# Optimization experiments

Measured on AMD Instinct MI355X. Metric: run time of the kernel, lower is better.

The kernel has to match this reference:

```python
import jax, jax.numpy as jnp
import numpy as np

B, N, G, H = 64, 1000, 500, 256
TANH_CLIP = 10.0


def setup_inputs() -> dict:
    key = jax.random.key(0)
    ks = jax.random.split(key, 8)
    embeddings = jax.random.normal(ks[0], (B, N, H), dtype=jnp.float32)
    dists = jax.random.uniform(ks[1], (B, N, N), dtype=jnp.float32)
    last_node = jax.random.randint(ks[2], (B, G), 0, N)
    visited = jax.random.uniform(ks[3], (B, G, N)) < 0.3
    group_ninf_mask = jnp.where(visited, -jnp.inf, 0.0).astype(jnp.float32)
    s = 1.0 / np.sqrt(H)
    Wq_graph = jax.random.normal(ks[4], (H, H), dtype=jnp.float32) * s
    Wq_first = jax.random.normal(ks[5], (H, H), dtype=jnp.float32) * s
    Wq_last = jax.random.normal(ks[6], (H, H), dtype=jnp.float32) * s
    W_visited = jax.random.normal(ks[7], (H, H), dtype=jnp.float32) * s
    return dict(embeddings=embeddings, dists=dists, last_node=last_node,
                group_ninf_mask=group_ninf_mask, Wq_graph=Wq_graph,
                Wq_first=Wq_first, Wq_last=Wq_last, W_visited=W_visited)


def reference(embeddings, dists, last_node, group_ninf_mask,
              Wq_graph, Wq_first, Wq_last, W_visited) -> jnp.ndarray:
    b, n, h = embeddings.shape
    g = last_node.shape[1]
    inv_sqrt_h = 1.0 / np.float32(np.sqrt(h))
    inv_sqrt_2 = np.float32(1.0 / np.sqrt(2.0))

    # reset(): graph query from mean-pooled embeddings  [B,1,H]
    q_graph = jnp.einsum('bih,oh->bio', embeddings.mean(axis=1, keepdims=True), Wq_graph)

    # gather last-node embeddings  [B,G,H]
    idx = jnp.broadcast_to(last_node[:, :, None], (b, g, h))
    last_emb = jnp.take_along_axis(embeddings, idx, axis=1)
    q_last = jnp.einsum('bgh,oh->bgo', last_emb, Wq_last)
    # first call: q_first built from the same last-node embedding
    q_first = jnp.einsum('bgh,oh->bgo', last_emb, Wq_first)

    # visited-set query: mask (-inf->1) @ embeddings / N, then linear
    mask_visited = jnp.where(jnp.isneginf(group_ninf_mask), 1.0, group_ninf_mask)
    pooled = jnp.einsum('bgn,bnh->bgh', mask_visited, embeddings) / np.float32(n)
    q_visited = jnp.einsum('bgh,oh->bgo', pooled, W_visited)

    # distances from last node to all nodes  [B,G,N]
    didx = jnp.broadcast_to(last_node[:, :, None], (b, g, n))
    distances = jnp.take_along_axis(dists, didx, axis=1)

    final_q = q_last + q_first + q_graph + q_visited  # [B,G,H]
    score = jnp.einsum('bgh,bnh->bgn', final_q, embeddings) * inv_sqrt_h - distances * inv_sqrt_2
    score_clipped = TANH_CLIP * jnp.tanh(score)
    mask_prob = jnp.where(jnp.isneginf(group_ninf_mask), -1e8, group_ninf_mask)
    return jax.nn.softmax(score_clipped + mask_prob, axis=-1)
```

## Files before the change

### kernel.cpp

```cpp
#include <hip/hip_runtime.h>
#include <hip/hip_fp16.h>
#include <math.h>

#define Bb 64
#define Nn 1000
#define Gg 500
#define Hh 256
#define GP 512
#define NP 1024

#define WS_QG   0u
#define WS_RS   16384u
#define WS_BM   49152u
#define WS_WC16 1097728u
#define WS_E16  1163264u
#define WS_T16  9355264u
#define WS_P16  17743872u
#define WS_F16  WS_T16
#define WS_PO   21938176u
#define WS_MP   38322176u

typedef __attribute__((ext_vector_type(8))) short short8;
typedef __attribute__((ext_vector_type(8))) _Float16 f16x8;
typedef __attribute__((ext_vector_type(4))) float f32x4;
typedef __attribute__((ext_vector_type(4))) unsigned short u16x4;

#define MFMAH(a,b,c) __builtin_amdgcn_mfma_f32_16x16x32_f16(a,b,c,0,0,0)
#define SW(row, chunk) (((row) << 6) + ((((chunk) ^ ((row) & 7))) << 3))

__device__ __forceinline__ unsigned short f16b(float v) {
  return __half_as_ushort(__float2half(v));
}

__global__ __launch_bounds__(256) void k_misc(const float* __restrict__ gm,
                                              const float* __restrict__ Wf,
                                              const float* __restrict__ Wl,
                                              const float* __restrict__ Wv,
                                              float* __restrict__ ws) {
  int bid = blockIdx.x, t = threadIdx.x;
  if (bid < 8192) {
    int w = t >> 6, l = t & 63;
    int row = bid * 4 + w;
    int b = row >> 9, g = row & 511;
    unsigned long long* dst = (unsigned long long*)((unsigned short*)(ws + WS_BM) + (size_t)row * 64);
    if (g < Gg) {
      const float* src = gm + ((size_t)b * Gg + g) * Nn;
#pragma unroll
      for (int i = 0; i < 16; ++i) {
        int n = i * 64 + l;
        bool bit = (n < Nn) ? (src[n] < -1e30f) : false;
        unsigned long long m = __ballot(bit);
        if (l == i) dst[i] = m;
      }
    } else {
      if (l < 16) dst[l] = 0ull;
    }
  } else if (bid < 8448) {
    int o = bid - 8192, k = t;
    unsigned short* wc = (unsigned short*)(ws + WS_WC16);
    wc[o*512 + k]       = f16b(Wv[o*Hh + k]);
    wc[o*512 + 256 + k] = f16b(Wl[o*Hh + k] + Wf[o*Hh + k]);
  } else {
    ws[WS_RS + (bid - 8448) * 256 + t] = 0.f;
  }
}

__global__ __launch_bounds__(256) void k_prep(const float* __restrict__ emb,
                                              float* __restrict__ ws) {
  __shared__ float tile[64][68];
  __shared__ float colsum[16][64];
  int nt = blockIdx.x, ht = blockIdx.y, b = blockIdx.z;
  int t = threadIdx.x;
  int c4 = (t & 15) * 4, r0 = t >> 4;
  int n0 = nt * 64, h0 = ht * 64;
  unsigned short* e16 = (unsigned short*)(ws + WS_E16);
  unsigned short* t16 = (unsigned short*)(ws + WS_T16);
  float cs0 = 0.f, cs1 = 0.f, cs2 = 0.f, cs3 = 0.f;
#pragma unroll
  for (int rr = 0; rr < 4; ++rr) {
    int r = r0 + rr * 16;
    int n = n0 + r;
    float4 v = {0.f, 0.f, 0.f, 0.f};
    if (n < Nn) {
      size_t idx = ((size_t)(b * Nn + n)) * Hh + h0 + c4;
      v = *(const float4*)(emb + idx);
      u16x4 e4 = { f16b(v.x), f16b(v.y), f16b(v.z), f16b(v.w) };
      *(u16x4*)(e16 + idx) = e4;
    }
    *(float4*)&tile[r][c4] = v;
    cs0 += v.x; cs1 += v.y; cs2 += v.z; cs3 += v.w;
  }
  colsum[r0][c4 + 0] = cs0; colsum[r0][c4 + 1] = cs1;
  colsum[r0][c4 + 2] = cs2; colsum[r0][c4 + 3] = cs3;
  __syncthreads();
  {
    int h_l = t >> 2, nseg = t & 3;
    short8 h8a, h8b;
#pragma unroll
    for (int i = 0; i < 16; ++i) {
      float v = tile[nseg * 16 + i][h_l];
      unsigned short hv = f16b(v);
      if (i < 8) h8a[i] = (short)hv;
      else       h8b[i-8] = (short)hv;
    }
    size_t base = ((size_t)(b * Hh + h0 + h_l)) * NP + n0 + nseg * 16;
    *(short8*)(t16 + base) = h8a; *(short8*)(t16 + base + 8) = h8b;
  }
  if (t < 64) {
    float s = 0.f;
#pragma unroll
    for (int i = 0; i < 16; ++i) s += colsum[i][t];
    ws[WS_MP + (((size_t)(b * Hh + h0 + t)) << 4) + nt] = s;
  }
}

__global__ __launch_bounds__(256) void k_qgraph(const float* __restrict__ Wg,
                                                float* __restrict__ ws) {
  __shared__ float mean[Hh];
  int b = blockIdx.x, t = threadIdx.x;
  {
    const float4* mp4 = (const float4*)(ws + WS_MP + (((size_t)(b * Hh + t)) << 4));
    float s = 0.f;
#pragma unroll
    for (int q = 0; q < 4; ++q) {
      float4 v = mp4[q];
      s += v.x + v.y + v.z + v.w;
    }
    mean[t] = s * (1.0f/Nn);
  }
  __syncthreads();
  const float4* wrow = (const float4*)(Wg + (size_t)t * Hh);
  float acc = 0.f;
#pragma unroll
  for (int h4 = 0; h4 < Hh/4; ++h4) {
    float4 w = wrow[h4];
    acc += mean[h4*4]*w.x + mean[h4*4+1]*w.y + mean[h4*4+2]*w.z + mean[h4*4+3]*w.w;
  }
  ws[WS_QG + b*Hh + t] = acc;
}

__global__ __launch_bounds__(256, 2) void k_pool(float* __restrict__ ws) {
  __shared__ __align__(16) unsigned short sT[128*64];
  int ht = blockIdx.x, gt = blockIdx.y, b = blockIdx.z;
  int t = threadIdx.x, w = t >> 6, lane = t & 63;
  int wh = w >> 1, wg = w & 1, l15 = lane & 15, lk = lane >> 4;
  const unsigned short* t16 = (const unsigned short*)(ws + WS_T16);
  const unsigned short* bmp = (const unsigned short*)(ws + WS_BM);
  unsigned short* p16 = (unsigned short*)(ws + WS_P16);
  int h0 = ht*128, g0 = gt*128;
  f32x4 acc[4][4] = {};
  const unsigned short* brow[4];
#pragma unroll
  for (int fn = 0; fn < 4; ++fn) {
    int g = g0 + wg*64 + fn*16 + l15; if (g > Gg-1) g = Gg-1;
    brow[fn] = bmp + ((size_t)(b*GP + g)) * 64;
  }
  int bitoff = (lk & 1) * 8;
  int srow = t >> 1, sc0 = (t & 1) * 4;
  size_t sbase = ((size_t)(b*Hh + h0 + srow)) * NP;
  for (int st = 0; st < 16; ++st) {
    int k0 = st * 64;
#pragma unroll
    for (int i = 0; i < 4; ++i) {
      int cc = sc0 + i;
      *(short8*)&sT[SW(srow, cc)] = *(const short8*)(t16 + sbase + k0 + cc*8);
    }
    __syncthreads();
#pragma unroll
    for (int kk = 0; kk < 64; kk += 32) {
      f16x8 ah[4], bmf[4];
#pragma unroll
      for (int fm = 0; fm < 4; ++fm)
        ah[fm] = *(const f16x8*)&sT[SW(wh*64 + fm*16 + l15, (kk>>3) + lk)];
#pragma unroll
      for (int fn = 0; fn < 4; ++fn) {
        unsigned c = brow[fn][((k0 + kk) >> 4) + (lk >> 1)];
        short8 bs;
#pragma unroll
        for (int i = 0; i < 8; ++i)
          bs[i] = ((c >> (bitoff + i)) & 1) ? (short)0x3C00 : (short)0;
        bmf[fn] = *(const f16x8*)&bs;
      }
#pragma unroll
      for (int fm = 0; fm < 4; ++fm)
#pragma unroll
        for (int fn = 0; fn < 4; ++fn)
          acc[fm][fn] = MFMAH(ah[fm], bmf[fn], acc[fm][fn]);
    }
    __syncthreads();
  }
#pragma unroll
  for (int fm = 0; fm < 4; ++fm)
#pragma unroll
    for (int fn = 0; fn < 4; ++fn) {
      int h = h0 + wh*64 + fm*16 + lk*4;
      int g = g0 + wg*64 + fn*16 + l15;
      u16x4 v4;
#pragma unroll
      for (int j = 0; j < 4; ++j) v4[j] = f16b(acc[fm][fn][j] * (1.0f/Nn));
      *(u16x4*)(p16 + ((size_t)(b*GP + g)) * Hh + h) = v4;
    }
}

__global__ __launch_bounds__(256, 2) void k_finalq(const int* __restrict__ last_node,
                                                   float* __restrict__ ws) {
  __shared__ __align__(16) unsigned short sA[128*64], sB[128*64];
  __shared__ int lL[128];
  int ot = blockIdx.x, gt = blockIdx.y, b = blockIdx.z;
  int t = threadIdx.x, w = t >> 6, lane = t & 63;
  int wo = w >> 1, wg = w & 1, l15 = lane & 15, lk = lane >> 4;
  const unsigned short* wc = (const unsigned short*)(ws + WS_WC16);
  const unsigned short* p16 = (const unsigned short*)(ws + WS_P16);
  const unsigned short* e16 = (const unsigned short*)(ws + WS_E16);
  unsigned short* f16 = (unsigned short*)(ws + WS_F16);
  int o0 = ot*128, g0 = gt*128;
  if (t < 128) lL[t] = last_node[b*Gg + ((g0 + t) < Gg ? (g0 + t) : Gg-1)];
  __syncthreads();
  f32x4 acc[4][4] = {};
  int srow = t >> 1, sc0 = (t & 1) * 4;
  size_t abase = ((size_t)(o0 + srow)) * 512;
  size_t pbase = ((size_t)(b*GP + g0 + srow)) * Hh;
  size_t lbase = ((size_t)(b*Nn + lL[srow])) * Hh;
  for (int st = 0; st < 8; ++st) {
    int k0 = st * 64;
#pragma unroll
    for (int i = 0; i < 4; ++i) {
      int cc = sc0 + i;
      int d = SW(srow, cc);
      *(short8*)&sA[d] = *(const short8*)(wc + abase + k0 + cc*8);
      if (k0 < 256)
        *(short8*)&sB[d] = *(const short8*)(p16 + pbase + k0 + cc*8);
      else
        *(short8*)&sB[d] = *(const short8*)(e16 + lbase + (k0 - 256) + cc*8);
    }
    __syncthreads();
#pragma unroll
    for (int kk = 0; kk < 64; kk += 32) {
      f16x8 a[4], bb[4];
#pragma unroll
      for (int fm = 0; fm < 4; ++fm)
        a[fm] = *(const f16x8*)&sA[SW(wo*64 + fm*16 + l15, (kk>>3) + lk)];
#pragma unroll
      for (int fn = 0; fn < 4; ++fn)
        bb[fn] = *(const f16x8*)&sB[SW(wg*64 + fn*16 + l15, (kk>>3) + lk)];
#pragma unroll
      for (int fm = 0; fm < 4; ++fm)
#pragma unroll
        for (int fn = 0; fn < 4; ++fn)
          acc[fm][fn] = MFMAH(a[fm], bb[fn], acc[fm][fn]);
    }
    __syncthreads();
  }
#pragma unroll
  for (int fm = 0; fm < 4; ++fm) {
    int o = o0 + wo*64 + fm*16 + lk*4;
    float4 qv = *(const float4*)(ws + WS_QG + b*Hh + o);
    float q4[4] = {qv.x, qv.y, qv.z, qv.w};
#pragma unroll
    for (int fn = 0; fn < 4; ++fn) {
      int g = g0 + wg*64 + fn*16 + l15;
      u16x4 v4;
#pragma unroll
      for (int j = 0; j < 4; ++j) v4[j] = f16b(acc[fm][fn][j] + q4[j]);
      *(u16x4*)(f16 + ((size_t)(b*GP + g)) * Hh + o) = v4;
    }
  }
}

__global__ __launch_bounds__(256, 4) void k_score(const float* __restrict__ dists,
                                                  const int* __restrict__ last_node,
                                                  float* __restrict__ ws) {
  __shared__ __align__(16) unsigned short sE[128*64], sF[128*64];
  __shared__ int lL[128];
  int id = blockIdx.x;
  int swz = ((id & 7) << 8) | (id >> 3);
  int gt = swz & 3, nt = (swz >> 2) & 7, b = swz >> 5;
  int t = threadIdx.x, w = t >> 6, lane = t & 63;
  int wn = w >> 1, wg = w & 1, l15 = lane & 15, lk = lane >> 4;
  const unsigned short* e16 = (const unsigned short*)(ws + WS_E16);
  const unsigned short* f16 = (const unsigned short*)(ws + WS_F16);
  const unsigned short* bmp = (const unsigned short*)(ws + WS_BM);
  unsigned short* po = (unsigned short*)(ws + WS_PO);
  float* rs = ws + WS_RS;
  int n0 = nt*128, g0 = gt*128;
  if (t < 128) lL[t] = last_node[b*Gg + ((g0 + t) < Gg ? (g0 + t) : Gg-1)];
  __syncthreads();
  f32x4 acc[4][4] = {};
  int srow = t >> 1, sc0 = (t & 1) * 4;
  int nr = n0 + srow; if (nr > Nn-1) nr = Nn-1;
  size_t ebase = ((size_t)(b*Nn + nr)) * Hh;
  size_t fbase = ((size_t)(b*GP + g0 + srow)) * Hh;
  for (int st = 0; st < 4; ++st) {
    int k0 = st * 64;
#pragma unroll
    for (int i = 0; i < 4; ++i) {
      int cc = sc0 + i;
      int d = SW(srow, cc);
      *(short8*)&sE[d] = *(const short8*)(e16 + ebase + k0 + cc*8);
      *(short8*)&sF[d] = *(const short8*)(f16 + fbase + k0 + cc*8);
    }
    __syncthreads();
#pragma unroll
    for (int kk = 0; kk < 64; kk += 32) {
      f16x8 a[4], bb[4];
#pragma unroll
      for (int fm = 0; fm < 4; ++fm)
        a[fm] = *(const f16x8*)&sE[SW(wn*64 + fm*16 + l15, (kk>>3) + lk)];
#pragma unroll
      for (int fn = 0; fn < 4; ++fn)
        bb[fn] = *(const f16x8*)&sF[SW(wg*64 + fn*16 + l15, (kk>>3) + lk)];
#pragma unroll
      for (int fm = 0; fm < 4; ++fm)
#pragma unroll
        for (int fn = 0; fn < 4; ++fn)
          acc[fm][fn] = MFMAH(a[fm], bb[fn], acc[fm][fn]);
    }
    __syncthreads();
  }
  const float c2 = 0.70710678118654752f;
  float rsum[4] = {0.f, 0.f, 0.f, 0.f};
#pragma unroll
  for (int fn = 0; fn < 4; ++fn) {
    int gl = wg*64 + fn*16 + l15;
    int g = g0 + gl;
    if (g < Gg) {
      int L = lL[gl];
      const float* drow = dists + ((size_t)(b*Nn + L)) * Nn;
      const unsigned short* bmr = bmp + ((size_t)(b*GP + g)) * 64;
      unsigned short* prow = po + ((size_t)(b*Gg + g)) * 1024;
#pragma unroll
      for (int fm = 0; fm < 4; ++fm) {
        int n = n0 + wn*64 + fm*16 + lk*4;
        if (n < Nn) {
          float4 d4 = *(const float4*)(drow + n);
          unsigned cb = bmr[n >> 4];
          int bo = n & 15;
          float dd[4] = {d4.x, d4.y, d4.z, d4.w};
          unsigned short h4[4];
#pragma unroll
          for (int j = 0; j < 4; ++j) {
            float s = fmaf(acc[fm][fn][j], 0.0625f, -dd[j] * c2);
            float e = __expf(-2.0f * fabsf(s));
            float r = __builtin_amdgcn_rcpf(1.0f + e);
            float m = fmaf(-20.0f, e * r, 10.0f);
            float parg = copysignf(m, s) - 10.0f;
            float p = ((cb >> (bo + j)) & 1) ? 0.f : __expf(parg);
            rsum[fn] += p;
            h4[j] = f16b(p);
          }
          uint2 u = { (unsigned)h4[0] | ((unsigned)h4[1] << 16),
                      (unsigned)h4[2] | ((unsigned)h4[3] << 16) };
          *(uint2*)(prow + n) = u;
        }
      }
    }
  }
#pragma unroll
  for (int fn = 0; fn < 4; ++fn) {
    rsum[fn] += __shfl_xor(rsum[fn], 16);
    rsum[fn] += __shfl_xor(rsum[fn], 32);
    int g = g0 + wg*64 + fn*16 + l15;
    if (lk == 0 && g < Gg) atomicAdd(rs + b*GP + g, rsum[fn]);
  }
}

__global__ __launch_bounds__(256) void k_norm(const float* __restrict__ ws,
                                              float* __restrict__ out) {
  int idx = blockIdx.x * 256 + threadIdx.x;
  int bg = idx / 125;
  int n = (idx - bg * 125) * 8;
  int b = bg / Gg, g = bg - b * Gg;
  const unsigned short* po = (const unsigned short*)(ws + WS_PO);
  float inv = 1.0f / ws[WS_RS + b*GP + g];
  uint4 u = *(const uint4*)(po + (size_t)bg * 1024 + n);
  float* orow = out + (size_t)bg * Nn + n;
  float4 o0, o1;
  o0.x = __half2float(__ushort_as_half((unsigned short)(u.x & 0xFFFF))) * inv;
  o0.y = __half2float(__ushort_as_half((unsigned short)(u.x >> 16))) * inv;
  o0.z = __half2float(__ushort_as_half((unsigned short)(u.y & 0xFFFF))) * inv;
  o0.w = __half2float(__ushort_as_half((unsigned short)(u.y >> 16))) * inv;
  o1.x = __half2float(__ushort_as_half((unsigned short)(u.z & 0xFFFF))) * inv;
  o1.y = __half2float(__ushort_as_half((unsigned short)(u.z >> 16))) * inv;
  o1.z = __half2float(__ushort_as_half((unsigned short)(u.w & 0xFFFF))) * inv;
  o1.w = __half2float(__ushort_as_half((unsigned short)(u.w >> 16))) * inv;
  *(float4*)orow = o0;
  *(float4*)(orow + 4) = o1;
}

extern "C" void kernel_launch(void* const* d_in, const int* in_sizes, int n_in,
                              void* d_out, int out_size, void* d_ws, size_t ws_size,
                              hipStream_t stream) {
  const float* emb       = (const float*)d_in[0];
  const float* dists     = (const float*)d_in[1];
  const int*   last_node = (const int*)d_in[2];
  const float* gm        = (const float*)d_in[3];
  const float* Wg        = (const float*)d_in[4];
  const float* Wf        = (const float*)d_in[5];
  const float* Wl        = (const float*)d_in[6];
  const float* Wv        = (const float*)d_in[7];
  float* out = (float*)d_out;
  float* ws  = (float*)d_ws;

  hipLaunchKernelGGL(k_misc,   dim3(8576),      dim3(256), 0, stream, gm, Wf, Wl, Wv, ws);
  hipLaunchKernelGGL(k_prep,   dim3(16,4,Bb),   dim3(256), 0, stream, emb, ws);
  hipLaunchKernelGGL(k_qgraph, dim3(Bb),        dim3(256), 0, stream, Wg, ws);
  hipLaunchKernelGGL(k_pool,   dim3(2,4,Bb),    dim3(256), 0, stream, ws);
  hipLaunchKernelGGL(k_finalq, dim3(2,4,Bb),    dim3(256), 0, stream, last_node, ws);
  hipLaunchKernelGGL(k_score,  dim3(2048),      dim3(256), 0, stream, dists, last_node, ws);
  hipLaunchKernelGGL(k_norm,   dim3(15625),     dim3(256), 0, stream, ws, out);
}
```

Measured before the change: 304.1 us.

## Fuse softmax normalization into score kernel and merge front-end kernels

The score kernel now gives each block full rows (32 groups across all 1000 nodes, in four passes). It keeps the fp16 probabilities in registers, reduces row sums in shared memory and writes the normalized float output directly. This removes the fp16 probability buffer round trip, the atomic row sums and the separate normalization kernel. The prep, mask-bitmap and weight-conversion kernels are merged into one launch, and the graph query is computed inside the final-query kernel, so the launch count drops from seven to four. In exchange the score blocks hold many registers, which limits occupancy, and the embedding tiles are reloaded for every 32-group block.

```diff
diff --git a/kernel.cpp b/kernel.cpp
--- a/kernel.cpp
+++ b/kernel.cpp
@@ -9,16 +9,13 @@
 #define GP 512
 #define NP 1024
 
-#define WS_QG   0u
-#define WS_RS   16384u
-#define WS_BM   49152u
-#define WS_WC16 1097728u
-#define WS_E16  1163264u
-#define WS_T16  9355264u
-#define WS_P16  17743872u
+#define WS_MP   0u
+#define WS_BM   262144u
+#define WS_WC16 1310720u
+#define WS_E16  1376256u
+#define WS_T16  9568256u
+#define WS_P16  17956864u
 #define WS_F16  WS_T16
-#define WS_PO   21938176u
-#define WS_MP   38322176u
 
 typedef __attribute__((ext_vector_type(8))) short short8;
 typedef __attribute__((ext_vector_type(8))) _Float16 f16x8;
@@ -31,16 +28,65 @@
 __device__ __forceinline__ unsigned short f16b(float v) {
   return __half_as_ushort(__float2half(v));
 }
-
-__global__ __launch_bounds__(256) void k_misc(const float* __restrict__ gm,
-                                              const float* __restrict__ Wf,
-                                              const float* __restrict__ Wl,
-                                              const float* __restrict__ Wv,
-                                              float* __restrict__ ws) {
+__device__ __forceinline__ float h2f(unsigned short u) {
+  return __half2float(__ushort_as_half(u));
+}
+
+__global__ __launch_bounds__(256) void k_front(const float* __restrict__ emb,
+                                               const float* __restrict__ gm,
+                                               const float* __restrict__ Wf,
+                                               const float* __restrict__ Wl,
+                                               const float* __restrict__ Wv,
+                                               float* __restrict__ ws) {
+  __shared__ float tile[64][68];
+  __shared__ float colsum[16][64];
   int bid = blockIdx.x, t = threadIdx.x;
-  if (bid < 8192) {
+  if (bid < 4096) {
+    int nt = bid & 15, ht = (bid >> 4) & 3, b = bid >> 6;
+    int c4 = (t & 15) * 4, r0 = t >> 4;
+    int n0 = nt * 64, h0 = ht * 64;
+    unsigned short* e16 = (unsigned short*)(ws + WS_E16);
+    unsigned short* t16 = (unsigned short*)(ws + WS_T16);
+    float cs0 = 0.f, cs1 = 0.f, cs2 = 0.f, cs3 = 0.f;
+#pragma unroll
+    for (int rr = 0; rr < 4; ++rr) {
+      int r = r0 + rr * 16;
+      int n = n0 + r;
+      float4 v = {0.f, 0.f, 0.f, 0.f};
+      if (n < Nn) {
+        size_t idx = ((size_t)(b * Nn + n)) * Hh + h0 + c4;
+        v = *(const float4*)(emb + idx);
+        u16x4 e4 = { f16b(v.x), f16b(v.y), f16b(v.z), f16b(v.w) };
+        *(u16x4*)(e16 + idx) = e4;
+      }
+      *(float4*)&tile[r][c4] = v;
+      cs0 += v.x; cs1 += v.y; cs2 += v.z; cs3 += v.w;
+    }
+    colsum[r0][c4 + 0] = cs0; colsum[r0][c4 + 1] = cs1;
+    colsum[r0][c4 + 2] = cs2; colsum[r0][c4 + 3] = cs3;
+    __syncthreads();
+    {
+      int h_l = t >> 2, nseg = t & 3;
+      short8 h8a, h8b;
+#pragma unroll
+      for (int i = 0; i < 16; ++i) {
+        float v = tile[nseg * 16 + i][h_l];
+        unsigned short hv = f16b(v);
+        if (i < 8) h8a[i] = (short)hv;
+        else       h8b[i-8] = (short)hv;
+      }
+      size_t base = ((size_t)(b * Hh + h0 + h_l)) * NP + n0 + nseg * 16;
+      *(short8*)(t16 + base) = h8a; *(short8*)(t16 + base + 8) = h8b;
+    }
+    if (t < 64) {
+      float s = 0.f;
+#pragma unroll
+      for (int i = 0; i < 16; ++i) s += colsum[i][t];
+      ws[WS_MP + (((size_t)(b * Hh + h0 + t)) << 4) + nt] = s;
+    }
+  } else if (bid < 12288) {
     int w = t >> 6, l = t & 63;
-    int row = bid * 4 + w;
+    int row = (bid - 4096) * 4 + w;
     int b = row >> 9, g = row & 511;
     unsigned long long* dst = (unsigned long long*)((unsigned short*)(ws + WS_BM) + (size_t)row * 64);
     if (g < Gg) {
@@ -55,88 +101,12 @@
     } else {
       if (l < 16) dst[l] = 0ull;
     }
-  } else if (bid < 8448) {
-    int o = bid - 8192, k = t;
+  } else {
+    int o = bid - 12288, k = t;
     unsigned short* wc = (unsigned short*)(ws + WS_WC16);
     wc[o*512 + k]       = f16b(Wv[o*Hh + k]);
     wc[o*512 + 256 + k] = f16b(Wl[o*Hh + k] + Wf[o*Hh + k]);
-  } else {
-    ws[WS_RS + (bid - 8448) * 256 + t] = 0.f;
-  }
-}
-
-__global__ __launch_bounds__(256) void k_prep(const float* __restrict__ emb,
-                                              float* __restrict__ ws) {
-  __shared__ float tile[64][68];
-  __shared__ float colsum[16][64];
-  int nt = blockIdx.x, ht = blockIdx.y, b = blockIdx.z;
-  int t = threadIdx.x;
-  int c4 = (t & 15) * 4, r0 = t >> 4;
-  int n0 = nt * 64, h0 = ht * 64;
-  unsigned short* e16 = (unsigned short*)(ws + WS_E16);
-  unsigned short* t16 = (unsigned short*)(ws + WS_T16);
-  float cs0 = 0.f, cs1 = 0.f, cs2 = 0.f, cs3 = 0.f;
-#pragma unroll
-  for (int rr = 0; rr < 4; ++rr) {
-    int r = r0 + rr * 16;
-    int n = n0 + r;
-    float4 v = {0.f, 0.f, 0.f, 0.f};
-    if (n < Nn) {
-      size_t idx = ((size_t)(b * Nn + n)) * Hh + h0 + c4;
-      v = *(const float4*)(emb + idx);
-      u16x4 e4 = { f16b(v.x), f16b(v.y), f16b(v.z), f16b(v.w) };
-      *(u16x4*)(e16 + idx) = e4;
-    }
-    *(float4*)&tile[r][c4] = v;
-    cs0 += v.x; cs1 += v.y; cs2 += v.z; cs3 += v.w;
-  }
-  colsum[r0][c4 + 0] = cs0; colsum[r0][c4 + 1] = cs1;
-  colsum[r0][c4 + 2] = cs2; colsum[r0][c4 + 3] = cs3;
-  __syncthreads();
-  {
-    int h_l = t >> 2, nseg = t & 3;
-    short8 h8a, h8b;
-#pragma unroll
-    for (int i = 0; i < 16; ++i) {
-      float v = tile[nseg * 16 + i][h_l];
-      unsigned short hv = f16b(v);
-      if (i < 8) h8a[i] = (short)hv;
-      else       h8b[i-8] = (short)hv;
-    }
-    size_t base = ((size_t)(b * Hh + h0 + h_l)) * NP + n0 + nseg * 16;
-    *(short8*)(t16 + base) = h8a; *(short8*)(t16 + base + 8) = h8b;
-  }
-  if (t < 64) {
-    float s = 0.f;
-#pragma unroll
-    for (int i = 0; i < 16; ++i) s += colsum[i][t];
-    ws[WS_MP + (((size_t)(b * Hh + h0 + t)) << 4) + nt] = s;
-  }
-}
-
-__global__ __launch_bounds__(256) void k_qgraph(const float* __restrict__ Wg,
-                                                float* __restrict__ ws) {
-  __shared__ float mean[Hh];
-  int b = blockIdx.x, t = threadIdx.x;
-  {
-    const float4* mp4 = (const float4*)(ws + WS_MP + (((size_t)(b * Hh + t)) << 4));
-    float s = 0.f;
-#pragma unroll
-    for (int q = 0; q < 4; ++q) {
-      float4 v = mp4[q];
-      s += v.x + v.y + v.z + v.w;
-    }
-    mean[t] = s * (1.0f/Nn);
-  }
-  __syncthreads();
-  const float4* wrow = (const float4*)(Wg + (size_t)t * Hh);
-  float acc = 0.f;
-#pragma unroll
-  for (int h4 = 0; h4 < Hh/4; ++h4) {
-    float4 w = wrow[h4];
-    acc += mean[h4*4]*w.x + mean[h4*4+1]*w.y + mean[h4*4+2]*w.z + mean[h4*4+3]*w.w;
-  }
-  ws[WS_QG + b*Hh + t] = acc;
+  }
 }
 
 __global__ __launch_bounds__(256, 2) void k_pool(float* __restrict__ ws) {
@@ -203,9 +173,12 @@
 }
 
 __global__ __launch_bounds__(256, 2) void k_finalq(const int* __restrict__ last_node,
+                                                   const float* __restrict__ Wg,
                                                    float* __restrict__ ws) {
   __shared__ __align__(16) unsigned short sA[128*64], sB[128*64];
   __shared__ int lL[128];
+  __shared__ float mean[256];
+  __shared__ float qv[128];
   int ot = blockIdx.x, gt = blockIdx.y, b = blockIdx.z;
   int t = threadIdx.x, w = t >> 6, lane = t & 63;
   int wo = w >> 1, wg = w & 1, l15 = lane & 15, lk = lane >> 4;
@@ -215,6 +188,27 @@
   unsigned short* f16 = (unsigned short*)(ws + WS_F16);
   int o0 = ot*128, g0 = gt*128;
   if (t < 128) lL[t] = last_node[b*Gg + ((g0 + t) < Gg ? (g0 + t) : Gg-1)];
+  {
+    const float4* mp4 = (const float4*)(ws + WS_MP + (((size_t)(b * Hh + t)) << 4));
+    float s = 0.f;
+#pragma unroll
+    for (int q = 0; q < 4; ++q) {
+      float4 v = mp4[q];
+      s += v.x + v.y + v.z + v.w;
+    }
+    mean[t] = s * (1.0f/Nn);
+  }
+  __syncthreads();
+  if (t < 128) {
+    const float4* wrow = (const float4*)(Wg + (size_t)(o0 + t) * Hh);
+    float a = 0.f;
+#pragma unroll
+    for (int h4 = 0; h4 < 64; ++h4) {
+      float4 wv = wrow[h4];
+      a += mean[h4*4]*wv.x + mean[h4*4+1]*wv.y + mean[h4*4+2]*wv.z + mean[h4*4+3]*wv.w;
+    }
+    qv[t] = a;
+  }
   __syncthreads();
   f32x4 acc[4][4] = {};
   int srow = t >> 1, sc0 = (t & 1) * 4;
@@ -253,138 +247,143 @@
   }
 #pragma unroll
   for (int fm = 0; fm < 4; ++fm) {
-    int o = o0 + wo*64 + fm*16 + lk*4;
-    float4 qv = *(const float4*)(ws + WS_QG + b*Hh + o);
-    float q4[4] = {qv.x, qv.y, qv.z, qv.w};
+    int ob = wo*64 + fm*16 + lk*4;
+    float q4[4] = { qv[ob+0], qv[ob+1], qv[ob+2], qv[ob+3] };
 #pragma unroll
     for (int fn = 0; fn < 4; ++fn) {
       int g = g0 + wg*64 + fn*16 + l15;
       u16x4 v4;
 #pragma unroll
       for (int j = 0; j < 4; ++j) v4[j] = f16b(acc[fm][fn][j] + q4[j]);
-      *(u16x4*)(f16 + ((size_t)(b*GP + g)) * Hh + o) = v4;
-    }
-  }
-}
-
-__global__ __launch_bounds__(256, 4) void k_score(const float* __restrict__ dists,
+      *(u16x4*)(f16 + ((size_t)(b*GP + g)) * Hh + o0 + ob) = v4;
+    }
+  }
+}
+
+__global__ __launch_bounds__(256, 2) void k_score(const float* __restrict__ dists,
                                                   const int* __restrict__ last_node,
-                                                  float* __restrict__ ws) {
-  __shared__ __align__(16) unsigned short sE[128*64], sF[128*64];
-  __shared__ int lL[128];
+                                                  float* __restrict__ ws,
+                                                  float* __restrict__ out) {
+  __shared__ __align__(16) unsigned short sE[256*64], sF[32*64];
+  __shared__ int lL[32];
+  __shared__ float rsp[4][32];
+  __shared__ float sInv[32];
   int id = blockIdx.x;
-  int swz = ((id & 7) << 8) | (id >> 3);
-  int gt = swz & 3, nt = (swz >> 2) & 7, b = swz >> 5;
+  int xcd = id & 7, seq = id >> 3;
+  int b = xcd * 8 + (seq >> 4);
+  int gt = seq & 15;
+  int g0 = gt * 32;
   int t = threadIdx.x, w = t >> 6, lane = t & 63;
-  int wn = w >> 1, wg = w & 1, l15 = lane & 15, lk = lane >> 4;
+  int l15 = lane & 15, lk = lane >> 4;
   const unsigned short* e16 = (const unsigned short*)(ws + WS_E16);
   const unsigned short* f16 = (const unsigned short*)(ws + WS_F16);
   const unsigned short* bmp = (const unsigned short*)(ws + WS_BM);
-  unsigned short* po = (unsigned short*)(ws + WS_PO);
-  float* rs = ws + WS_RS;
-  int n0 = nt*128, g0 = gt*128;
-  if (t < 128) lL[t] = last_node[b*Gg + ((g0 + t) < Gg ? (g0 + t) : Gg-1)];
-  __syncthreads();
-  f32x4 acc[4][4] = {};
-  int srow = t >> 1, sc0 = (t & 1) * 4;
-  int nr = n0 + srow; if (nr > Nn-1) nr = Nn-1;
-  size_t ebase = ((size_t)(b*Nn + nr)) * Hh;
-  size_t fbase = ((size_t)(b*GP + g0 + srow)) * Hh;
-  for (int st = 0; st < 4; ++st) {
-    int k0 = st * 64;
-#pragma unroll
-    for (int i = 0; i < 4; ++i) {
-      int cc = sc0 + i;
-      int d = SW(srow, cc);
-      *(short8*)&sE[d] = *(const short8*)(e16 + ebase + k0 + cc*8);
-      *(short8*)&sF[d] = *(const short8*)(f16 + fbase + k0 + cc*8);
-    }
-    __syncthreads();
-#pragma unroll
-    for (int kk = 0; kk < 64; kk += 32) {
-      f16x8 a[4], bb[4];
-#pragma unroll
-      for (int fm = 0; fm < 4; ++fm)
-        a[fm] = *(const f16x8*)&sE[SW(wn*64 + fm*16 + l15, (kk>>3) + lk)];
-#pragma unroll
-      for (int fn = 0; fn < 4; ++fn)
-        bb[fn] = *(const f16x8*)&sF[SW(wg*64 + fn*16 + l15, (kk>>3) + lk)];
-#pragma unroll
-      for (int fm = 0; fm < 4; ++fm)
-#pragma unroll
-        for (int fn = 0; fn < 4; ++fn)
-          acc[fm][fn] = MFMAH(a[fm], bb[fn], acc[fm][fn]);
-    }
-    __syncthreads();
-  }
+  if (t < 32) lL[t] = last_node[b*Gg + ((g0 + t) < Gg ? (g0 + t) : Gg-1)];
   const float c2 = 0.70710678118654752f;
-  float rsum[4] = {0.f, 0.f, 0.f, 0.f};
-#pragma unroll
-  for (int fn = 0; fn < 4; ++fn) {
-    int gl = wg*64 + fn*16 + l15;
-    int g = g0 + gl;
-    if (g < Gg) {
-      int L = lL[gl];
-      const float* drow = dists + ((size_t)(b*Nn + L)) * Nn;
-      const unsigned short* bmr = bmp + ((size_t)(b*GP + g)) * 64;
-      unsigned short* prow = po + ((size_t)(b*Gg + g)) * 1024;
-#pragma unroll
-      for (int fm = 0; fm < 4; ++fm) {
-        int n = n0 + wn*64 + fm*16 + lk*4;
-        if (n < Nn) {
-          float4 d4 = *(const float4*)(drow + n);
-          unsigned cb = bmr[n >> 4];
-          int bo = n & 15;
-          float dd[4] = {d4.x, d4.y, d4.z, d4.w};
-          unsigned short h4[4];
-#pragma unroll
-          for (int j = 0; j < 4; ++j) {
-            float s = fmaf(acc[fm][fn][j], 0.0625f, -dd[j] * c2);
-            float e = __expf(-2.0f * fabsf(s));
-            float r = __builtin_amdgcn_rcpf(1.0f + e);
-            float m = fmaf(-20.0f, e * r, 10.0f);
-            float parg = copysignf(m, s) - 10.0f;
-            float p = ((cb >> (bo + j)) & 1) ? 0.f : __expf(parg);
-            rsum[fn] += p;
-            h4[j] = f16b(p);
+  float rsum[2] = {0.f, 0.f};
+  unsigned pst[4][4][2][2];
+#pragma unroll
+  for (int pass = 0; pass < 4; ++pass) {
+    f32x4 acc[4][2] = {};
+    for (int st = 0; st < 4; ++st) {
+      int k0 = st * 64;
+      __syncthreads();
+#pragma unroll
+      for (int i = 0; i < 8; ++i) {
+        int c = i * 256 + t;
+        int row = c >> 3, ch = c & 7;
+        int n = pass*256 + row; if (n > Nn-1) n = Nn-1;
+        *(short8*)&sE[SW(row, ch)] =
+            *(const short8*)(e16 + ((size_t)(b*Nn + n))*Hh + k0 + ch*8);
+      }
+      {
+        int row = t >> 3, ch = t & 7;
+        *(short8*)&sF[SW(row, ch)] =
+            *(const short8*)(f16 + ((size_t)(b*GP + g0 + row))*Hh + k0 + ch*8);
+      }
+      __syncthreads();
+#pragma unroll
+      for (int kk = 0; kk < 64; kk += 32) {
+        f16x8 a[4], bb[2];
+#pragma unroll
+        for (int fm = 0; fm < 4; ++fm)
+          a[fm] = *(const f16x8*)&sE[SW(w*64 + fm*16 + l15, (kk>>3) + lk)];
+#pragma unroll
+        for (int fn = 0; fn < 2; ++fn)
+          bb[fn] = *(const f16x8*)&sF[SW(fn*16 + l15, (kk>>3) + lk)];
+#pragma unroll
+        for (int fm = 0; fm < 4; ++fm)
+#pragma unroll
+          for (int fn = 0; fn < 2; ++fn)
+            acc[fm][fn] = MFMAH(a[fm], bb[fn], acc[fm][fn]);
+      }
+    }
+#pragma unroll
+    for (int fm = 0; fm < 4; ++fm) {
+      int n = pass*256 + w*64 + fm*16 + lk*4;
+      if (n < Nn) {
+#pragma unroll
+        for (int fn = 0; fn < 2; ++fn) {
+          int gl = fn*16 + l15, g = g0 + gl;
+          if (g < Gg) {
+            int L = lL[gl];
+            float4 d4 = *(const float4*)(dists + ((size_t)(b*Nn + L))*Nn + n);
+            unsigned cb = bmp[((size_t)(b*GP + g))*64 + (n >> 4)];
+            int bo = n & 15;
+            float dd[4] = {d4.x, d4.y, d4.z, d4.w};
+            unsigned short h4[4];
+#pragma unroll
+            for (int j = 0; j < 4; ++j) {
+              float s = fmaf(acc[fm][fn][j], 0.0625f, -dd[j] * c2);
+              float e = __expf(-2.0f * fabsf(s));
+              float r = __builtin_amdgcn_rcpf(1.0f + e);
+              float m = fmaf(-20.0f, e * r, 10.0f);
+              float parg = copysignf(m, s) - 10.0f;
+              float p = ((cb >> (bo + j)) & 1) ? 0.f : __expf(parg);
+              rsum[fn] += p;
+              h4[j] = f16b(p);
+            }
+            pst[pass][fm][fn][0] = (unsigned)h4[0] | ((unsigned)h4[1] << 16);
+            pst[pass][fm][fn][1] = (unsigned)h4[2] | ((unsigned)h4[3] << 16);
           }
-          uint2 u = { (unsigned)h4[0] | ((unsigned)h4[1] << 16),
-                      (unsigned)h4[2] | ((unsigned)h4[3] << 16) };
-          *(uint2*)(prow + n) = u;
         }
       }
     }
   }
 #pragma unroll
-  for (int fn = 0; fn < 4; ++fn) {
+  for (int fn = 0; fn < 2; ++fn) {
     rsum[fn] += __shfl_xor(rsum[fn], 16);
     rsum[fn] += __shfl_xor(rsum[fn], 32);
-    int g = g0 + wg*64 + fn*16 + l15;
-    if (lk == 0 && g < Gg) atomicAdd(rs + b*GP + g, rsum[fn]);
-  }
-}
-
-__global__ __launch_bounds__(256) void k_norm(const float* __restrict__ ws,
-                                              float* __restrict__ out) {
-  int idx = blockIdx.x * 256 + threadIdx.x;
-  int bg = idx / 125;
-  int n = (idx - bg * 125) * 8;
-  int b = bg / Gg, g = bg - b * Gg;
-  const unsigned short* po = (const unsigned short*)(ws + WS_PO);
-  float inv = 1.0f / ws[WS_RS + b*GP + g];
-  uint4 u = *(const uint4*)(po + (size_t)bg * 1024 + n);
-  float* orow = out + (size_t)bg * Nn + n;
-  float4 o0, o1;
-  o0.x = __half2float(__ushort_as_half((unsigned short)(u.x & 0xFFFF))) * inv;
-  o0.y = __half2float(__ushort_as_half((unsigned short)(u.x >> 16))) * inv;
-  o0.z = __half2float(__ushort_as_half((unsigned short)(u.y & 0xFFFF))) * inv;
-  o0.w = __half2float(__ushort_as_half((unsigned short)(u.y >> 16))) * inv;
-  o1.x = __half2float(__ushort_as_half((unsigned short)(u.z & 0xFFFF))) * inv;
-  o1.y = __half2float(__ushort_as_half((unsigned short)(u.z >> 16))) * inv;
-  o1.z = __half2float(__ushort_as_half((unsigned short)(u.w & 0xFFFF))) * inv;
-  o1.w = __half2float(__ushort_as_half((unsigned short)(u.w >> 16))) * inv;
-  *(float4*)orow = o0;
-  *(float4*)(orow + 4) = o1;
+  }
+  if (lk == 0) { rsp[w][l15] = rsum[0]; rsp[w][16 + l15] = rsum[1]; }
+  __syncthreads();
+  if (t < 32) {
+    float s = rsp[0][t] + rsp[1][t] + rsp[2][t] + rsp[3][t];
+    sInv[t] = 1.0f / s;
+  }
+  __syncthreads();
+#pragma unroll
+  for (int pass = 0; pass < 4; ++pass)
+#pragma unroll
+    for (int fm = 0; fm < 4; ++fm) {
+      int n = pass*256 + w*64 + fm*16 + lk*4;
+      if (n < Nn) {
+#pragma unroll
+        for (int fn = 0; fn < 2; ++fn) {
+          int gl = fn*16 + l15, g = g0 + gl;
+          if (g < Gg) {
+            float iv = sInv[gl];
+            unsigned u0 = pst[pass][fm][fn][0], u1 = pst[pass][fm][fn][1];
+            float4 o4;
+            o4.x = h2f((unsigned short)(u0 & 0xFFFF)) * iv;
+            o4.y = h2f((unsigned short)(u0 >> 16)) * iv;
+            o4.z = h2f((unsigned short)(u1 & 0xFFFF)) * iv;
+            o4.w = h2f((unsigned short)(u1 >> 16)) * iv;
+            *(float4*)(out + ((size_t)(b*Gg + g))*Nn + n) = o4;
+          }
+        }
+      }
+    }
 }
 
 extern "C" void kernel_launch(void* const* d_in, const int* in_sizes, int n_in,
@@ -401,11 +400,8 @@
   float* out = (float*)d_out;
   float* ws  = (float*)d_ws;
 
-  hipLaunchKernelGGL(k_misc,   dim3(8576),      dim3(256), 0, stream, gm, Wf, Wl, Wv, ws);
-  hipLaunchKernelGGL(k_prep,   dim3(16,4,Bb),   dim3(256), 0, stream, emb, ws);
-  hipLaunchKernelGGL(k_qgraph, dim3(Bb),        dim3(256), 0, stream, Wg, ws);
+  hipLaunchKernelGGL(k_front,  dim3(12544),     dim3(256), 0, stream, emb, gm, Wf, Wl, Wv, ws);
   hipLaunchKernelGGL(k_pool,   dim3(2,4,Bb),    dim3(256), 0, stream, ws);
-  hipLaunchKernelGGL(k_finalq, dim3(2,4,Bb),    dim3(256), 0, stream, last_node, ws);
-  hipLaunchKernelGGL(k_score,  dim3(2048),      dim3(256), 0, stream, dists, last_node, ws);
-  hipLaunchKernelGGL(k_norm,   dim3(15625),     dim3(256), 0, stream, ws, out);
-}
+  hipLaunchKernelGGL(k_finalq, dim3(2,4,Bb),    dim3(256), 0, stream, last_node, Wg, ws);
+  hipLaunchKernelGGL(k_score,  dim3(1024),      dim3(256), 0, stream, dists, last_node, ws, out);
+}
```

Result: slower. 312.6 us (+2.8%).

## Merge prep and misc kernels, fold q_graph computation into finalq

Applied to the files above, without the earlier changes.

Merges the embedding conversion/transpose kernel into the mask-bitmap/weight-prep kernel as one launch with branch-selected block roles. Removes the separate q_graph kernel by having each finalq block compute the mean and its 128-wide slice of the graph query in shared memory. This cuts two kernel launches and their serialization gaps. In exchange, q_graph is recomputed redundantly across g-tiles (4x per batch), and finalq carries extra shared memory and a prologue delay.

```diff
diff --git a/kernel.cpp b/kernel.cpp
--- a/kernel.cpp
+++ b/kernel.cpp
@@ -9,16 +9,15 @@
 #define GP 512
 #define NP 1024
 
-#define WS_QG   0u
-#define WS_RS   16384u
-#define WS_BM   49152u
-#define WS_WC16 1097728u
-#define WS_E16  1163264u
-#define WS_T16  9355264u
-#define WS_P16  17743872u
+#define WS_MP   0u
+#define WS_RS   262144u
+#define WS_BM   294912u
+#define WS_WC16 1343488u
+#define WS_E16  1409024u
+#define WS_T16  9601024u
+#define WS_P16  17989632u
 #define WS_F16  WS_T16
-#define WS_PO   21938176u
-#define WS_MP   38322176u
+#define WS_PO   22183936u
 
 typedef __attribute__((ext_vector_type(8))) short short8;
 typedef __attribute__((ext_vector_type(8))) _Float16 f16x8;
@@ -31,16 +30,65 @@
 __device__ __forceinline__ unsigned short f16b(float v) {
   return __half_as_ushort(__float2half(v));
 }
-
-__global__ __launch_bounds__(256) void k_misc(const float* __restrict__ gm,
-                                              const float* __restrict__ Wf,
-                                              const float* __restrict__ Wl,
-                                              const float* __restrict__ Wv,
-                                              float* __restrict__ ws) {
+__device__ __forceinline__ float h2f(unsigned short u) {
+  return __half2float(__ushort_as_half(u));
+}
+
+__global__ __launch_bounds__(256) void k_front(const float* __restrict__ emb,
+                                               const float* __restrict__ gm,
+                                               const float* __restrict__ Wf,
+                                               const float* __restrict__ Wl,
+                                               const float* __restrict__ Wv,
+                                               float* __restrict__ ws) {
+  __shared__ float tile[64][68];
+  __shared__ float colsum[16][64];
   int bid = blockIdx.x, t = threadIdx.x;
-  if (bid < 8192) {
+  if (bid < 4096) {
+    int nt = bid & 15, ht = (bid >> 4) & 3, b = bid >> 6;
+    int c4 = (t & 15) * 4, r0 = t >> 4;
+    int n0 = nt * 64, h0 = ht * 64;
+    unsigned short* e16 = (unsigned short*)(ws + WS_E16);
+    unsigned short* t16 = (unsigned short*)(ws + WS_T16);
+    float cs0 = 0.f, cs1 = 0.f, cs2 = 0.f, cs3 = 0.f;
+#pragma unroll
+    for (int rr = 0; rr < 4; ++rr) {
+      int r = r0 + rr * 16;
+      int n = n0 + r;
+      float4 v = {0.f, 0.f, 0.f, 0.f};
+      if (n < Nn) {
+        size_t idx = ((size_t)(b * Nn + n)) * Hh + h0 + c4;
+        v = *(const float4*)(emb + idx);
+        u16x4 e4 = { f16b(v.x), f16b(v.y), f16b(v.z), f16b(v.w) };
+        *(u16x4*)(e16 + idx) = e4;
+      }
+      *(float4*)&tile[r][c4] = v;
+      cs0 += v.x; cs1 += v.y; cs2 += v.z; cs3 += v.w;
+    }
+    colsum[r0][c4 + 0] = cs0; colsum[r0][c4 + 1] = cs1;
+    colsum[r0][c4 + 2] = cs2; colsum[r0][c4 + 3] = cs3;
+    __syncthreads();
+    {
+      int h_l = t >> 2, nseg = t & 3;
+      short8 h8a, h8b;
+#pragma unroll
+      for (int i = 0; i < 16; ++i) {
+        float v = tile[nseg * 16 + i][h_l];
+        unsigned short hv = f16b(v);
+        if (i < 8) h8a[i] = (short)hv;
+        else       h8b[i-8] = (short)hv;
+      }
+      size_t base = ((size_t)(b * Hh + h0 + h_l)) * NP + n0 + nseg * 16;
+      *(short8*)(t16 + base) = h8a; *(short8*)(t16 + base + 8) = h8b;
+    }
+    if (t < 64) {
+      float s = 0.f;
+#pragma unroll
+      for (int i = 0; i < 16; ++i) s += colsum[i][t];
+      ws[WS_MP + (((size_t)(b * Hh + h0 + t)) << 4) + nt] = s;
+    }
+  } else if (bid < 12288) {
     int w = t >> 6, l = t & 63;
-    int row = bid * 4 + w;
+    int row = (bid - 4096) * 4 + w;
     int b = row >> 9, g = row & 511;
     unsigned long long* dst = (unsigned long long*)((unsigned short*)(ws + WS_BM) + (size_t)row * 64);
     if (g < Gg) {
@@ -55,88 +103,14 @@
     } else {
       if (l < 16) dst[l] = 0ull;
     }
-  } else if (bid < 8448) {
-    int o = bid - 8192, k = t;
+  } else if (bid < 12544) {
+    int o = bid - 12288, k = t;
     unsigned short* wc = (unsigned short*)(ws + WS_WC16);
     wc[o*512 + k]       = f16b(Wv[o*Hh + k]);
     wc[o*512 + 256 + k] = f16b(Wl[o*Hh + k] + Wf[o*Hh + k]);
   } else {
-    ws[WS_RS + (bid - 8448) * 256 + t] = 0.f;
-  }
-}
-
-__global__ __launch_bounds__(256) void k_prep(const float* __restrict__ emb,
-                                              float* __restrict__ ws) {
-  __shared__ float tile[64][68];
-  __shared__ float colsum[16][64];
-  int nt = blockIdx.x, ht = blockIdx.y, b = blockIdx.z;
-  int t = threadIdx.x;
-  int c4 = (t & 15) * 4, r0 = t >> 4;
-  int n0 = nt * 64, h0 = ht * 64;
-  unsigned short* e16 = (unsigned short*)(ws + WS_E16);
-  unsigned short* t16 = (unsigned short*)(ws + WS_T16);
-  float cs0 = 0.f, cs1 = 0.f, cs2 = 0.f, cs3 = 0.f;
-#pragma unroll
-  for (int rr = 0; rr < 4; ++rr) {
-    int r = r0 + rr * 16;
-    int n = n0 + r;
-    float4 v = {0.f, 0.f, 0.f, 0.f};
-    if (n < Nn) {
-      size_t idx = ((size_t)(b * Nn + n)) * Hh + h0 + c4;
-      v = *(const float4*)(emb + idx);
-      u16x4 e4 = { f16b(v.x), f16b(v.y), f16b(v.z), f16b(v.w) };
-      *(u16x4*)(e16 + idx) = e4;
-    }
-    *(float4*)&tile[r][c4] = v;
-    cs0 += v.x; cs1 += v.y; cs2 += v.z; cs3 += v.w;
-  }
-  colsum[r0][c4 + 0] = cs0; colsum[r0][c4 + 1] = cs1;
-  colsum[r0][c4 + 2] = cs2; colsum[r0][c4 + 3] = cs3;
-  __syncthreads();
-  {
-    int h_l = t >> 2, nseg = t & 3;
-    short8 h8a, h8b;
-#pragma unroll
-    for (int i = 0; i < 16; ++i) {
-      float v = tile[nseg * 16 + i][h_l];
-      unsigned short hv = f16b(v);
-      if (i < 8) h8a[i] = (short)hv;
-      else       h8b[i-8] = (short)hv;
-    }
-    size_t base = ((size_t)(b * Hh + h0 + h_l)) * NP + n0 + nseg * 16;
-    *(short8*)(t16 + base) = h8a; *(short8*)(t16 + base + 8) = h8b;
-  }
-  if (t < 64) {
-    float s = 0.f;
-#pragma unroll
-    for (int i = 0; i < 16; ++i) s += colsum[i][t];
-    ws[WS_MP + (((size_t)(b * Hh + h0 + t)) << 4) + nt] = s;
-  }
-}
-
-__global__ __launch_bounds__(256) void k_qgraph(const float* __restrict__ Wg,
-                                                float* __restrict__ ws) {
-  __shared__ float mean[Hh];
-  int b = blockIdx.x, t = threadIdx.x;
-  {
-    const float4* mp4 = (const float4*)(ws + WS_MP + (((size_t)(b * Hh + t)) << 4));
-    float s = 0.f;
-#pragma unroll
-    for (int q = 0; q < 4; ++q) {
-      float4 v = mp4[q];
-      s += v.x + v.y + v.z + v.w;
-    }
-    mean[t] = s * (1.0f/Nn);
-  }
-  __syncthreads();
-  const float4* wrow = (const float4*)(Wg + (size_t)t * Hh);
-  float acc = 0.f;
-#pragma unroll
-  for (int h4 = 0; h4 < Hh/4; ++h4) {
-    float4 w = wrow[h4];
-    acc += mean[h4*4]*w.x + mean[h4*4+1]*w.y + mean[h4*4+2]*w.z + mean[h4*4+3]*w.w;
-  }
-  ws[WS_QG + b*Hh + t] = acc;
+    ws[WS_RS + (bid - 12544) * 256 + t] = 0.f;
+  }
 }
 
 __global__ __launch_bounds__(256, 2) void k_pool(float* __restrict__ ws) {
@@ -203,9 +177,12 @@
 }
 
 __global__ __launch_bounds__(256, 2) void k_finalq(const int* __restrict__ last_node,
+                                                   const float* __restrict__ Wg,
                                                    float* __restrict__ ws) {
   __shared__ __align__(16) unsigned short sA[128*64], sB[128*64];
   __shared__ int lL[128];
+  __shared__ float mean[256];
+  __shared__ float qv[128];
   int ot = blockIdx.x, gt = blockIdx.y, b = blockIdx.z;
   int t = threadIdx.x, w = t >> 6, lane = t & 63;
   int wo = w >> 1, wg = w & 1, l15 = lane & 15, lk = lane >> 4;
@@ -215,6 +192,27 @@
   unsigned short* f16 = (unsigned short*)(ws + WS_F16);
   int o0 = ot*128, g0 = gt*128;
   if (t < 128) lL[t] = last_node[b*Gg + ((g0 + t) < Gg ? (g0 + t) : Gg-1)];
+  {
+    const float4* mp4 = (const float4*)(ws + WS_MP + (((size_t)(b * Hh + t)) << 4));
+    float s = 0.f;
+#pragma unroll
+    for (int q = 0; q < 4; ++q) {
+      float4 v = mp4[q];
+      s += v.x + v.y + v.z + v.w;
+    }
+    mean[t] = s * (1.0f/Nn);
+  }
+  __syncthreads();
+  if (t < 128) {
+    const float4* wrow = (const float4*)(Wg + (size_t)(o0 + t) * Hh);
+    float a = 0.f;
+#pragma unroll
+    for (int h4 = 0; h4 < 64; ++h4) {
+      float4 wv = wrow[h4];
+      a += mean[h4*4]*wv.x + mean[h4*4+1]*wv.y + mean[h4*4+2]*wv.z + mean[h4*4+3]*wv.w;
+    }
+    qv[t] = a;
+  }
   __syncthreads();
   f32x4 acc[4][4] = {};
   int srow = t >> 1, sc0 = (t & 1) * 4;
@@ -253,16 +251,15 @@
   }
 #pragma unroll
   for (int fm = 0; fm < 4; ++fm) {
-    int o = o0 + wo*64 + fm*16 + lk*4;
-    float4 qv = *(const float4*)(ws + WS_QG + b*Hh + o);
-    float q4[4] = {qv.x, qv.y, qv.z, qv.w};
+    int ob = wo*64 + fm*16 + lk*4;
+    float q4[4] = { qv[ob+0], qv[ob+1], qv[ob+2], qv[ob+3] };
 #pragma unroll
     for (int fn = 0; fn < 4; ++fn) {
       int g = g0 + wg*64 + fn*16 + l15;
       u16x4 v4;
 #pragma unroll
       for (int j = 0; j < 4; ++j) v4[j] = f16b(acc[fm][fn][j] + q4[j]);
-      *(u16x4*)(f16 + ((size_t)(b*GP + g)) * Hh + o) = v4;
+      *(u16x4*)(f16 + ((size_t)(b*GP + g)) * Hh + o0 + ob) = v4;
     }
   }
 }
@@ -375,14 +372,14 @@
   uint4 u = *(const uint4*)(po + (size_t)bg * 1024 + n);
   float* orow = out + (size_t)bg * Nn + n;
   float4 o0, o1;
-  o0.x = __half2float(__ushort_as_half((unsigned short)(u.x & 0xFFFF))) * inv;
-  o0.y = __half2float(__ushort_as_half((unsigned short)(u.x >> 16))) * inv;
-  o0.z = __half2float(__ushort_as_half((unsigned short)(u.y & 0xFFFF))) * inv;
-  o0.w = __half2float(__ushort_as_half((unsigned short)(u.y >> 16))) * inv;
-  o1.x = __half2float(__ushort_as_half((unsigned short)(u.z & 0xFFFF))) * inv;
-  o1.y = __half2float(__ushort_as_half((unsigned short)(u.z >> 16))) * inv;
-  o1.z = __half2float(__ushort_as_half((unsigned short)(u.w & 0xFFFF))) * inv;
-  o1.w = __half2float(__ushort_as_half((unsigned short)(u.w >> 16))) * inv;
+  o0.x = h2f((unsigned short)(u.x & 0xFFFF)) * inv;
+  o0.y = h2f((unsigned short)(u.x >> 16)) * inv;
+  o0.z = h2f((unsigned short)(u.y & 0xFFFF)) * inv;
+  o0.w = h2f((unsigned short)(u.y >> 16)) * inv;
+  o1.x = h2f((unsigned short)(u.z & 0xFFFF)) * inv;
+  o1.y = h2f((unsigned short)(u.z >> 16)) * inv;
+  o1.z = h2f((unsigned short)(u.w & 0xFFFF)) * inv;
+  o1.w = h2f((unsigned short)(u.w >> 16)) * inv;
   *(float4*)orow = o0;
   *(float4*)(orow + 4) = o1;
 }
@@ -401,11 +398,9 @@
   float* out = (float*)d_out;
   float* ws  = (float*)d_ws;
 
-  hipLaunchKernelGGL(k_misc,   dim3(8576),      dim3(256), 0, stream, gm, Wf, Wl, Wv, ws);
-  hipLaunchKernelGGL(k_prep,   dim3(16,4,Bb),   dim3(256), 0, stream, emb, ws);
-  hipLaunchKernelGGL(k_qgraph, dim3(Bb),        dim3(256), 0, stream, Wg, ws);
+  hipLaunchKernelGGL(k_front,  dim3(12672),     dim3(256), 0, stream, emb, gm, Wf, Wl, Wv, ws);
   hipLaunchKernelGGL(k_pool,   dim3(2,4,Bb),    dim3(256), 0, stream, ws);
-  hipLaunchKernelGGL(k_finalq, dim3(2,4,Bb),    dim3(256), 0, stream, last_node, ws);
+  hipLaunchKernelGGL(k_finalq, dim3(2,4,Bb),    dim3(256), 0, stream, last_node, Wg, ws);
   hipLaunchKernelGGL(k_score,  dim3(2048),      dim3(256), 0, stream, dists, last_node, ws);
   hipLaunchKernelGGL(k_norm,   dim3(15625),     dim3(256), 0, stream, ws, out);
 }
```

After: 300.3 us. Within noise of the previous version (-1.3%).
